# Kernel tuning notes

Hardware: AMD Instinct MI355X
Metric: run time of the kernel (lower is better)

## Reference

```python
import jax, jax.numpy as jnp
import numpy as np

IN_FEATURES_A = 256
IN_FEATURES_B = 256


def setup_inputs() -> dict:
    key = jax.random.key(0)
    # x: [2, batch, features]; x[0] -> x_a, x[1] -> x_b
    x = jax.random.normal(key, (2, 2048, 256), dtype=jnp.float32)
    return {"x": x}


def reference(x) -> jnp.ndarray:
    # Split and truncate exactly like the torch module
    x_a = x[0][:, :IN_FEATURES_A]  # [B, A]
    x_b = x[1][:, :IN_FEATURES_B]  # [B, Kb]
    bsz = x_a.shape[0]
    # torch.kron of two 1-D vectors == flattened outer product (a-major order)
    y = jnp.einsum("ba,bk->bak", x_a, x_b).reshape(bsz, IN_FEATURES_A * IN_FEATURES_B)
    return jax.nn.softmax(y, axis=1)
```

## Files before the change

### kernel.cpp

```cpp
#include <hip/hip_runtime.h>


constexpr int FA   = 256;
constexpr int FB   = 256;
constexpr int ROWS = 2048;

typedef float f32x4 __attribute__((ext_vector_type(4)));

__global__ __launch_bounds__(256) void krone_softmax_kernel(
    const float* __restrict__ x, float* __restrict__ out) {
  const int row = blockIdx.x;
  const int tid = threadIdx.x;

  const float* __restrict__ xa = x + (size_t)row * FA;
  const float* __restrict__ xb = x + (size_t)ROWS * FA + (size_t)row * FB;

  __shared__ float sa[FA];
  __shared__ float sb[FB];
  __shared__ float wred[4][4];
  __shared__ float wsum[4];

  const float a = xa[tid];
  const float b = xb[tid];
  sa[tid] = a;
  sb[tid] = b;

  float maxa = a, mina = a, maxb = b, minb = b;
#pragma unroll
  for (int off = 32; off > 0; off >>= 1) {
    maxa = fmaxf(maxa, __shfl_xor(maxa, off));
    mina = fminf(mina, __shfl_xor(mina, off));
    maxb = fmaxf(maxb, __shfl_xor(maxb, off));
    minb = fminf(minb, __shfl_xor(minb, off));
  }
  const int wid = tid >> 6;
  if ((tid & 63) == 0) {
    wred[wid][0] = maxa; wred[wid][1] = mina;
    wred[wid][2] = maxb; wred[wid][3] = minb;
  }
  __syncthreads();
  const float MA = fmaxf(fmaxf(wred[0][0], wred[1][0]), fmaxf(wred[2][0], wred[3][0]));
  const float mA = fminf(fminf(wred[0][1], wred[1][1]), fminf(wred[2][1], wred[3][1]));
  const float MB = fmaxf(fmaxf(wred[0][2], wred[1][2]), fmaxf(wred[2][2], wred[3][2]));
  const float mB = fminf(fminf(wred[0][3], wred[1][3]), fminf(wred[2][3], wred[3][3]));
  const float M = fmaxf(fmaxf(MA * MB, MA * mB), fmaxf(mA * MB, mA * mB));

  constexpr float LOG2E = 1.4426950408889634f;
  const float mM2 = -M * LOG2E;

  const float bs = b * LOG2E;
  float s0 = 0.f, s1 = 0.f, s2 = 0.f, s3 = 0.f;
#pragma unroll 4
  for (int i = 0; i < FA; i += 4) {
    s0 += __builtin_amdgcn_exp2f(fmaf(sa[i + 0], bs, mM2));
    s1 += __builtin_amdgcn_exp2f(fmaf(sa[i + 1], bs, mM2));
    s2 += __builtin_amdgcn_exp2f(fmaf(sa[i + 2], bs, mM2));
    s3 += __builtin_amdgcn_exp2f(fmaf(sa[i + 3], bs, mM2));
  }
  float s = (s0 + s1) + (s2 + s3);
#pragma unroll
  for (int off = 32; off > 0; off >>= 1) s += __shfl_xor(s, off);
  if ((tid & 63) == 0) wsum[wid] = s;
  __syncthreads();
  const float sum = (wsum[0] + wsum[1]) + (wsum[2] + wsum[3]);

  const float C = mM2 - __builtin_amdgcn_logf(sum);

  float* __restrict__ orow = out + (size_t)row * (FA * FB);
  const int lane = tid & 63;
  const int j = lane * 4;
  f32x4 b4 = *reinterpret_cast<const f32x4*>(&sb[j]);
  b4 *= LOG2E;
  float* __restrict__ oseg = orow + wid * (64 * FB);
#pragma unroll 8
  for (int it = 0; it < 64; ++it) {
    const float av = sa[wid * 64 + it];
    f32x4 v;
    v.x = __builtin_amdgcn_exp2f(fmaf(av, b4.x, C));
    v.y = __builtin_amdgcn_exp2f(fmaf(av, b4.y, C));
    v.z = __builtin_amdgcn_exp2f(fmaf(av, b4.z, C));
    v.w = __builtin_amdgcn_exp2f(fmaf(av, b4.w, C));
    __builtin_nontemporal_store(v, reinterpret_cast<f32x4*>(&oseg[it * FB + j]));
  }
}

extern "C" void kernel_launch(void* const* d_in, const int* in_sizes, int n_in,
                              void* d_out, int out_size, void* d_ws, size_t ws_size,
                              hipStream_t stream) {
  const float* x = (const float*)d_in[0];
  float* out = (float*)d_out;
  krone_softmax_kernel<<<ROWS, 256, 0, stream>>>(x, out);
}
```

Baseline: 104.0 us.

## Split softmax into reduction kernel and pure-store kernel via workspace

```diff
diff --git a/kernel.cpp b/kernel.cpp
--- a/kernel.cpp
+++ b/kernel.cpp
@@ -4,11 +4,12 @@
 constexpr int FA   = 256;
 constexpr int FB   = 256;
 constexpr int ROWS = 2048;
+constexpr float LOG2E = 1.4426950408889634f;
 
 typedef float f32x4 __attribute__((ext_vector_type(4)));
 
-__global__ __launch_bounds__(256) void krone_softmax_kernel(
-    const float* __restrict__ x, float* __restrict__ out) {
+__global__ __launch_bounds__(256) void krone_reduce_kernel(
+    const float* __restrict__ x, float* __restrict__ Cbuf) {
   const int row = blockIdx.x;
   const int tid = threadIdx.x;
 
@@ -16,14 +17,12 @@
   const float* __restrict__ xb = x + (size_t)ROWS * FA + (size_t)row * FB;
 
   __shared__ float sa[FA];
-  __shared__ float sb[FB];
   __shared__ float wred[4][4];
   __shared__ float wsum[4];
 
   const float a = xa[tid];
   const float b = xb[tid];
   sa[tid] = a;
-  sb[tid] = b;
 
   float maxa = a, mina = a, maxb = b, minb = b;
 #pragma unroll
@@ -44,8 +43,6 @@
   const float MB = fmaxf(fmaxf(wred[0][2], wred[1][2]), fmaxf(wred[2][2], wred[3][2]));
   const float mB = fminf(fminf(wred[0][3], wred[1][3]), fminf(wred[2][3], wred[3][3]));
   const float M = fmaxf(fmaxf(MA * MB, MA * mB), fmaxf(mA * MB, mA * mB));
-
-  constexpr float LOG2E = 1.4426950408889634f;
   const float mM2 = -M * LOG2E;
 
   const float bs = b * LOG2E;
@@ -62,10 +59,91 @@
   for (int off = 32; off > 0; off >>= 1) s += __shfl_xor(s, off);
   if ((tid & 63) == 0) wsum[wid] = s;
   __syncthreads();
+  if (tid == 0) {
+    const float sum = (wsum[0] + wsum[1]) + (wsum[2] + wsum[3]);
+    Cbuf[row] = mM2 - __builtin_amdgcn_logf(sum);
+  }
+}
+
+__global__ __launch_bounds__(256) void krone_store_kernel(
+    const float* __restrict__ x, const float* __restrict__ Cbuf,
+    float* __restrict__ out) {
+  const int row = blockIdx.x;
+  const int tid = threadIdx.x;
+  const int wid = tid >> 6;
+  const int lane = tid & 63;
+
+  const float* __restrict__ xa = x + (size_t)row * FA;
+  const float* __restrict__ xb = x + (size_t)ROWS * FA + (size_t)row * FB;
+
+  const float aval = xa[wid * 64 + lane];
+  const int j = lane * 4;
+  f32x4 b4 = *reinterpret_cast<const f32x4*>(&xb[j]);
+  b4 *= LOG2E;
+  const float C = Cbuf[row];
+
+  float* __restrict__ oseg = out + (size_t)row * (FA * FB) + wid * (64 * FB);
+#pragma unroll 8
+  for (int it = 0; it < 64; ++it) {
+    const float av = __shfl(aval, it);
+    f32x4 v;
+    v.x = __builtin_amdgcn_exp2f(fmaf(av, b4.x, C));
+    v.y = __builtin_amdgcn_exp2f(fmaf(av, b4.y, C));
+    v.z = __builtin_amdgcn_exp2f(fmaf(av, b4.z, C));
+    v.w = __builtin_amdgcn_exp2f(fmaf(av, b4.w, C));
+    __builtin_nontemporal_store(v, reinterpret_cast<f32x4*>(&oseg[it * FB + j]));
+  }
+}
+
+__global__ __launch_bounds__(256) void krone_fused_kernel(
+    const float* __restrict__ x, float* __restrict__ out) {
+  const int row = blockIdx.x;
+  const int tid = threadIdx.x;
+  const float* __restrict__ xa = x + (size_t)row * FA;
+  const float* __restrict__ xb = x + (size_t)ROWS * FA + (size_t)row * FB;
+  __shared__ float sa[FA];
+  __shared__ float sb[FB];
+  __shared__ float wred[4][4];
+  __shared__ float wsum[4];
+  const float a = xa[tid];
+  const float b = xb[tid];
+  sa[tid] = a; sb[tid] = b;
+  float maxa = a, mina = a, maxb = b, minb = b;
+#pragma unroll
+  for (int off = 32; off > 0; off >>= 1) {
+    maxa = fmaxf(maxa, __shfl_xor(maxa, off));
+    mina = fminf(mina, __shfl_xor(mina, off));
+    maxb = fmaxf(maxb, __shfl_xor(maxb, off));
+    minb = fminf(minb, __shfl_xor(minb, off));
+  }
+  const int wid = tid >> 6;
+  if ((tid & 63) == 0) {
+    wred[wid][0] = maxa; wred[wid][1] = mina;
+    wred[wid][2] = maxb; wred[wid][3] = minb;
+  }
+  __syncthreads();
+  const float MA = fmaxf(fmaxf(wred[0][0], wred[1][0]), fmaxf(wred[2][0], wred[3][0]));
+  const float mA = fminf(fminf(wred[0][1], wred[1][1]), fminf(wred[2][1], wred[3][1]));
+  const float MB = fmaxf(fmaxf(wred[0][2], wred[1][2]), fmaxf(wred[2][2], wred[3][2]));
+  const float mB = fminf(fminf(wred[0][3], wred[1][3]), fminf(wred[2][3], wred[3][3]));
+  const float M = fmaxf(fmaxf(MA * MB, MA * mB), fmaxf(mA * MB, mA * mB));
+  const float mM2 = -M * LOG2E;
+  const float bs = b * LOG2E;
+  float s0 = 0.f, s1 = 0.f, s2 = 0.f, s3 = 0.f;
+#pragma unroll 4
+  for (int i = 0; i < FA; i += 4) {
+    s0 += __builtin_amdgcn_exp2f(fmaf(sa[i + 0], bs, mM2));
+    s1 += __builtin_amdgcn_exp2f(fmaf(sa[i + 1], bs, mM2));
+    s2 += __builtin_amdgcn_exp2f(fmaf(sa[i + 2], bs, mM2));
+    s3 += __builtin_amdgcn_exp2f(fmaf(sa[i + 3], bs, mM2));
+  }
+  float s = (s0 + s1) + (s2 + s3);
+#pragma unroll
+  for (int off = 32; off > 0; off >>= 1) s += __shfl_xor(s, off);
+  if ((tid & 63) == 0) wsum[wid] = s;
+  __syncthreads();
   const float sum = (wsum[0] + wsum[1]) + (wsum[2] + wsum[3]);
-
   const float C = mM2 - __builtin_amdgcn_logf(sum);
-
   float* __restrict__ orow = out + (size_t)row * (FA * FB);
   const int lane = tid & 63;
   const int j = lane * 4;
@@ -89,5 +167,11 @@
                               hipStream_t stream) {
   const float* x = (const float*)d_in[0];
   float* out = (float*)d_out;
-  krone_softmax_kernel<<<ROWS, 256, 0, stream>>>(x, out);
+  if (ws_size >= ROWS * sizeof(float)) {
+    float* Cbuf = (float*)d_ws;
+    krone_reduce_kernel<<<ROWS, 256, 0, stream>>>(x, Cbuf);
+    krone_store_kernel<<<ROWS, 256, 0, stream>>>(x, Cbuf, out);
+  } else {
+    krone_fused_kernel<<<ROWS, 256, 0, stream>>>(x, out);
+  }
 }
```

Result: slower. 116.7 us (+12.3%).
